# Kernel optimization log

Measured on AMD Instinct MI355X. Metric: run time of the kernel, lower is better.

The kernel has to match this reference:

```python
import jax, jax.numpy as jnp
import numpy as np

EPS = 1e-12  # F.normalize default eps


def setup_inputs() -> dict:
    key = jax.random.key(0)
    x = jax.random.normal(key, (10000, 512), dtype=jnp.float32)
    return {"x": x, "k": 9}


def reference(x, k):
    # F.normalize(x, p=2, dim=0): L2-normalize each feature column over points
    col_norm = jnp.sqrt(jnp.sum(x * x, axis=0, keepdims=True))  # [1, D]
    xn = x / jnp.maximum(col_norm, EPS)                          # [N, D]

    # pairwise squared euclidean distance: ||xi||^2 - 2 xi.xj + ||xj||^2
    sq = jnp.sum(xn * xn, axis=-1, keepdims=True)                # [N, 1]
    dist = sq - 2.0 * (xn @ xn.T) + sq.T                          # [N, N]

    # k nearest neighbors = top-k of negative distance
    _, nn_idx = jax.lax.top_k(-dist, k)                           # [N, k] int32

    n = x.shape[0]
    center_idx = jnp.broadcast_to(jnp.arange(n, dtype=nn_idx.dtype)[:, None], (n, k))
    edge_idx = jnp.stack((nn_idx, center_idx), axis=0)            # [2, N, k]
    return edge_idx
```

## Files before the change

### kernel.cpp

```cpp
#include <hip/hip_runtime.h>
#include <math.h>

#define DD 512
#define NBLKA 400

#define PM 128
#define PN 128
#define KB 64
#define CSPLIT 6
#define NC 12
#define PBUF 32
#define PBSTRIDE 36
#define NCTOT (CSPLIT*NC)
#define KOUTMAX 16
#define RS_MARGIN 2e-4f

typedef __attribute__((ext_vector_type(8))) short bf16x8;
typedef __attribute__((ext_vector_type(4))) float f32x4;

static __device__ __forceinline__ unsigned short f2bf(float f) {
    unsigned u = __float_as_uint(f);
    u += 0x7fff + ((u >> 16) & 1);
    return (unsigned short)(u >> 16);
}

__global__ void colsum_partial(const float* __restrict__ x, double* __restrict__ partial,
                               int N, int rows_per_block) {
    int b = blockIdx.x;
    int t = threadIdx.x;
    int r0 = b * rows_per_block;
    int r1 = min(r0 + rows_per_block, N);
    double s0 = 0.0, s1 = 0.0;
    for (int r = r0; r < r1; ++r) {
        float v0 = x[(size_t)r * DD + t];
        float v1 = x[(size_t)r * DD + t + 256];
        s0 += (double)v0 * (double)v0;
        s1 += (double)v1 * (double)v1;
    }
    partial[(size_t)b * DD + t]       = s0;
    partial[(size_t)b * DD + t + 256] = s1;
}

__global__ void colnorm_finish(const double* __restrict__ partial, double* __restrict__ rn,
                               double* __restrict__ w, int nblk) {
    int c = threadIdx.x;
    double s = 0.0;
    for (int b = 0; b < nblk; ++b) s += partial[(size_t)b * DD + c];
    double n = fmax(sqrt(s), 1e-12);
    double r = 1.0 / n;
    rn[c]  = r;
    w[c]   = r * r;
}

__global__ void row_sq(const float* __restrict__ x, const double* __restrict__ rn,
                       double* __restrict__ sq, float* __restrict__ sqf,
                       unsigned short* __restrict__ xnbf, int N) {
    int i = blockIdx.x;
    int t = threadIdx.x;
    double a0 = (double)x[(size_t)i * DD + t]       * rn[t];
    double a1 = (double)x[(size_t)i * DD + t + 256] * rn[t + 256];
    xnbf[(size_t)i * DD + t]       = f2bf((float)a0);
    xnbf[(size_t)i * DD + t + 256] = f2bf((float)a1);
    double local = a0 * a0 + a1 * a1;
    __shared__ double red[256];
    red[t] = local;
    __syncthreads();
    for (int off = 128; off > 0; off >>= 1) {
        if (t < off) red[t] += red[t + off];
        __syncthreads();
    }
    if (t == 0) { sq[i] = red[0]; sqf[i] = (float)red[0]; }
}

__global__ __launch_bounds__(256, 2) void gemm_prefilter(
    const unsigned short* __restrict__ xnbf,
    const float* __restrict__ sqf, int* __restrict__ cand, float* __restrict__ cands,
    int N, int ntileM, int ntileN)
{
    __shared__ __align__(16) unsigned char lds_raw[65536];
    __shared__ float sqi_s[PM];
    __shared__ float sqj_s[PN];
    __shared__ float thr_s[PM];
    __shared__ int   cnt_s[PM];
    __shared__ int   flag_s;

    float (*Bsc)[PBSTRIDE] = (float (*)[PBSTRIDE]) lds_raw;
    int   (*Bid)[PBSTRIDE] = (int   (*)[PBSTRIDE]) (lds_raw + 32768);

    const int bid   = blockIdx.x;
    const int q     = bid & 7;
    const int s     = bid >> 3;
    const int ridx  = s / CSPLIT;
    const int split = s - ridx * CSPLIT;
    const int rowb  = q + 8 * ridx;
    if (rowb >= ntileM) return;
    const int row0  = rowb * PM;

    const int t      = threadIdx.x;
    const int lane15 = t & 15;
    const int quad   = (t >> 4) & 3;
    const int wave   = t >> 6;
    const int wr     = (wave >> 1) * 64;
    const int wc     = (wave & 1) * 64;

    if (t == 0) flag_s = 0;
    if (t < PM) {
        int i = row0 + t;
        sqi_s[t] = (i < N) ? sqf[i] : 0.f;
        thr_s[t] = __builtin_inff();
        cnt_s[t] = 0;
    }

    float ls[NC];
    int   li[NC];
#pragma unroll
    for (int m = 0; m < NC; ++m) { ls[m] = __builtin_inff(); li[m] = 0x7fffffff; }

    f32x4 acc[4][4];

    for (int tile = split; tile < ntileN; tile += CSPLIT) {
        int col0 = tile * PN;

        if (t < PN) {
            int j = col0 + t;
            sqj_s[t] = (j < N) ? sqf[j] : __builtin_inff();
        }
        __syncthreads();

#pragma unroll
        for (int mt = 0; mt < 4; ++mt)
#pragma unroll
            for (int nt = 0; nt < 4; ++nt)
                acc[mt][nt] = (f32x4){0.f, 0.f, 0.f, 0.f};

        auto STAGE = [&](int kc, int buf) {
#pragma unroll
            for (int l = 0; l < 4; ++l) {
                int e    = t + l * 256;
                int half = e >> 9;
                int re   = e & 511;
                int row  = re >> 2;
                int c    = re & 3;
                size_t gA = (size_t)(row0 + row) * DD + kc + half * 32 + c * 8;
                __builtin_amdgcn_global_load_lds(
                    (const unsigned int*)(xnbf + gA),
                    (unsigned int*)(lds_raw + (size_t)buf * 16384 + (size_t)e * 16), 16, 0, 0);
                size_t gB = (size_t)(col0 + row) * DD + kc + half * 32 + c * 8;
                __builtin_amdgcn_global_load_lds(
                    (const unsigned int*)(xnbf + gB),
                    (unsigned int*)(lds_raw + 32768 + (size_t)buf * 16384 + (size_t)e * 16), 16, 0, 0);
            }
        };

        STAGE(0, 0);
#pragma unroll 1
        for (int cc = 0; cc < 8; ++cc) {
            if (cc < 7) {
                STAGE((cc + 1) * KB, (cc + 1) & 1);
                __builtin_amdgcn_sched_barrier(0);
                asm volatile("s_waitcnt vmcnt(8)" ::: "memory");
            } else {
                __builtin_amdgcn_sched_barrier(0);
                asm volatile("s_waitcnt vmcnt(0)" ::: "memory");
            }
            __builtin_amdgcn_s_barrier();
            __builtin_amdgcn_sched_barrier(0);

            const unsigned short (*Ab)[PM][32] =
                (const unsigned short (*)[PM][32])(lds_raw + (size_t)(cc & 1) * 16384);
            const unsigned short (*Bb)[PN][32] =
                (const unsigned short (*)[PN][32])(lds_raw + 32768 + (size_t)(cc & 1) * 16384);
#pragma unroll
            for (int ks = 0; ks < 2; ++ks) {
                bf16x8 af[4], bfg[4];
#pragma unroll
                for (int mt = 0; mt < 4; ++mt)
                    af[mt] = *(const bf16x8*)&Ab[ks][wr + mt * 16 + lane15][quad * 8];
#pragma unroll
                for (int nt = 0; nt < 4; ++nt)
                    bfg[nt] = *(const bf16x8*)&Bb[ks][wc + nt * 16 + lane15][quad * 8];
#pragma unroll
                for (int mt = 0; mt < 4; ++mt)
#pragma unroll
                    for (int nt = 0; nt < 4; ++nt)
                        acc[mt][nt] = __builtin_amdgcn_mfma_f32_16x16x32_bf16(
                            af[mt], bfg[nt], acc[mt][nt], 0, 0, 0);
            }
            __builtin_amdgcn_sched_barrier(0);
            __builtin_amdgcn_s_barrier();
        }

#pragma unroll
        for (int mt = 0; mt < 4; ++mt)
#pragma unroll
            for (int nt = 0; nt < 4; ++nt)
#pragma unroll
                for (int reg = 0; reg < 4; ++reg) {
                    int rl = wr + mt * 16 + quad * 4 + reg;
                    int cl = wc + nt * 16 + lane15;
                    float g = acc[mt][nt][reg];
                    acc[mt][nt][reg] = (sqi_s[rl] - 2.f * g) + sqj_s[cl];
                }

        bool tile_edge = (col0 + PN > N);
        unsigned long long done = 0ull;
        for (;;) {
#pragma unroll
            for (int mt = 0; mt < 4; ++mt)
#pragma unroll
                for (int reg = 0; reg < 4; ++reg) {
                    const unsigned long long gb =
                        (0x1111ull << reg) << (mt * 16);
                    int rl = wr + mt * 16 + quad * 4 + reg;
                    float th = thr_s[rl];
                    float gmin = fminf(fminf(acc[mt][0][reg], acc[mt][1][reg]),
                                       fminf(acc[mt][2][reg], acc[mt][3][reg]));
                    if (!tile_edge && gmin > th) { done |= gb; continue; }
                    if ((done & gb) == gb) continue;
#pragma unroll
                    for (int nt = 0; nt < 4; ++nt) {
                        const unsigned long long bit = 1ull << (mt * 16 + nt * 4 + reg);
                        if (!(done & bit)) {
                            float sv = acc[mt][nt][reg];
                            int   j  = col0 + wc + nt * 16 + lane15;
                            if (j < N && sv <= th) {
                                int pos = atomicAdd(&cnt_s[rl], 1);
                                if (pos < PBUF) {
                                    Bsc[rl][pos] = sv;
                                    Bid[rl][pos] = j;
                                    done |= bit;
                                }
                            } else {
                                done |= bit;
                            }
                        }
                    }
                }
            if (done != ~0ull) flag_s = 1;
            __syncthreads();
            if (t < PM) {
                int c = cnt_s[t];
                if (c > PBUF) c = PBUF;
                cnt_s[t] = 0;
                for (int m0 = 0; m0 < c; m0 += 4) {
                    float4 s4 = *(const float4*)&Bsc[t][m0];
                    int4   j4 = *(const int4*)&Bid[t][m0];
#pragma unroll
                    for (int e = 0; e < 4; ++e) {
                        if (m0 + e >= c) break;
                        float sv = (e == 0) ? s4.x : (e == 1) ? s4.y : (e == 2) ? s4.z : s4.w;
                        int   j  = (e == 0) ? j4.x : (e == 1) ? j4.y : (e == 2) ? j4.z : j4.w;
                        if (sv < ls[NC - 1] || (sv == ls[NC - 1] && j < li[NC - 1])) {
                            float cs = sv; int cj = j;
#pragma unroll
                            for (int p = 0; p < NC; ++p) {
                                bool lt = (cs < ls[p]) || (cs == ls[p] && cj < li[p]);
                                float ts = ls[p]; int tj = li[p];
                                if (lt) { ls[p] = cs; li[p] = cj; cs = ts; cj = tj; }
                            }
                        }
                    }
                }
                thr_s[t] = ls[NC - 1];
            }
            __syncthreads();
            int go = flag_s;
            __syncthreads();
            if (t == 0) flag_s = 0;
            __syncthreads();
            if (!go) break;
        }
    }
    if (t < PM) {
        int i = row0 + t;
        if (i < N) {
#pragma unroll
            for (int m = 0; m < NC; ++m) {
                cand [(size_t)i * NCTOT + split * NC + m] = li[m];
                cands[(size_t)i * NCTOT + split * NC + m] = ls[m];
            }
        }
    }
}

__global__ __launch_bounds__(256) void rescore_topk(
    const float* __restrict__ x, const double* __restrict__ w,
    const double* __restrict__ sq, const int* __restrict__ cand,
    const float* __restrict__ cands, int* __restrict__ out, int N, int k)
{
    __shared__ float Ssc[4][NCTOT];
    int lane = threadIdx.x & 63;
    int wid  = threadIdx.x >> 6;
    int i = blockIdx.x * 4 + wid;
    if (i >= N) return;

    size_t base = (size_t)i * NCTOT;
    Ssc[wid][lane] = cands[base + lane];
    if (lane < NCTOT - 64) Ssc[wid][64 + lane] = cands[base + 64 + lane];

    float p0 = Ssc[wid][lane];
    float p1 = Ssc[wid][64 + (lane & 7)];
    int c0 = 0, c1 = 0;
    for (int m = 0; m < NCTOT; ++m) {
        float s = Ssc[wid][m];
        c0 += (s <= p0); c1 += (s <= p1);
    }
    float best = __builtin_inff();
    if (c0 >= k) best = p0;
    if (c1 >= k && p1 < best) best = p1;
#pragma unroll
    for (int off = 32; off > 0; off >>= 1)
        best = fminf(best, __shfl_xor(best, off, 64));
    float cut = best + RS_MARGIN;

    double aw[8];
#pragma unroll
    for (int c = 0; c < 8; ++c) {
        int d = lane + 64 * c;
        aw[c] = (double)x[(size_t)i * DD + d] * w[d];
    }
    double sqi = sq[i];

    double bs[KOUTMAX];
    int    bj[KOUTMAX];
    for (int r = 0; r < k; ++r) { bs[r] = __builtin_inf(); bj[r] = 0x7fffffff; }

    int pend = -1;
    for (int m = 0; m <= NCTOT; ++m) {
        int j1cand = -1;
        if (m < NCTOT) {
            if (Ssc[wid][m] > cut) continue;
            j1cand = cand[base + m];
            if (pend < 0) { pend = j1cand; continue; }
        } else if (pend < 0) {
            break;
        }
        int j0 = pend, j1 = j1cand;
        pend = -1;
        const float* q0 = &x[(size_t)j0 * DD + lane];
        const float* q1 = (j1 >= 0) ? &x[(size_t)j1 * DD + lane] : q0;
        float v0[8], v1[8];
#pragma unroll
        for (int c = 0; c < 8; ++c) v0[c] = q0[64 * c];
#pragma unroll
        for (int c = 0; c < 8; ++c) v1[c] = q1[64 * c];
        double d0 = 0.0, d1 = 0.0;
#pragma unroll
        for (int c = 0; c < 8; ++c) d0 = fma(aw[c], (double)v0[c], d0);
#pragma unroll
        for (int c = 0; c < 8; ++c) d1 = fma(aw[c], (double)v1[c], d1);
#pragma unroll
        for (int off = 32; off > 0; off >>= 1) {
            d0 += __shfl_xor(d0, off, 64);
            d1 += __shfl_xor(d1, off, 64);
        }
        double s0 = (sqi - 2.0 * d0) + sq[j0];
        double s1 = (j1 >= 0) ? (sqi - 2.0 * d1) + sq[j1] : __builtin_inf();
#pragma unroll 1
        for (int pick = 0; pick < 2; ++pick) {
            double sv = pick ? s1 : s0;
            int    j  = pick ? j1 : j0;
            if (j < 0) continue;
            if (sv < bs[k - 1] || (sv == bs[k - 1] && j < bj[k - 1])) {
                int pos = k - 1;
                while (pos > 0) {
                    double ps = bs[pos - 1]; int pj = bj[pos - 1];
                    if (!(sv < ps || (sv == ps && j < pj))) break;
                    bs[pos] = ps; bj[pos] = pj;
                    --pos;
                }
                bs[pos] = sv; bj[pos] = j;
            }
        }
    }
    if (lane == 0) {
        for (int r = 0; r < k; ++r) {
            out[(size_t)i * k + r]                 = bj[r];
            out[(size_t)N * k + (size_t)i * k + r] = i;
        }
    }
}

extern "C" void kernel_launch(void* const* d_in, const int* in_sizes, int n_in,
                              void* d_out, int out_size, void* d_ws, size_t ws_size,
                              hipStream_t stream) {
    const float* x = (const float*)d_in[0];
    int N = in_sizes[0] / DD;
    int k = out_size / (2 * N);
    if (k > KOUTMAX) k = KOUTMAX;

    char* ws = (char*)d_ws;
    double*         partial = (double*)ws;
    double*         rn      = (double*)(ws + 1638400);
    double*         w       = (double*)(ws + 1642496);
    double*         sq      = (double*)(ws + 1646592);
    float*          sqf     = (float*) (ws + 1726592);
    unsigned short* xnbf    = (unsigned short*)(ws + 1766592);
    int*            cand    = (int*)   (ws + 12006592);
    float*          cands   = (float*) (ws + 14886592);

    int rpb = (N + NBLKA - 1) / NBLKA;
    hipLaunchKernelGGL(colsum_partial, dim3(NBLKA), dim3(256), 0, stream, x, partial, N, rpb);
    hipLaunchKernelGGL(colnorm_finish, dim3(1), dim3(512), 0, stream, partial, rn, w, NBLKA);
    hipLaunchKernelGGL(row_sq, dim3(N), dim3(256), 0, stream, x, rn, sq, sqf, xnbf, N);

    int ntileM = (N + PM - 1) / PM;
    int ntileN = (N + PN - 1) / PN;
    int rows_per_xcd = (ntileM + 7) / 8;
    int nblk = 8 * rows_per_xcd * CSPLIT;
    hipLaunchKernelGGL(gemm_prefilter, dim3(nblk), dim3(256), 0, stream,
                       xnbf, sqf, cand, cands, N, ntileM, ntileN);

    hipLaunchKernelGGL(rescore_topk, dim3((N + 3) / 4), dim3(256), 0, stream,
                       x, w, sq, cand, cands, (int*)d_out, N, k);
}
```

Before: 774.0 us.

## Keep per-row top-candidate lists in registers with transposed MFMA tiling

Restructures the GEMM prefilter so each wave owns 32 query rows across all 128 columns, swapping MFMA operand order so each lane holds distance values for a single query row. Candidates are inserted directly into per-lane register top-NC lists and then merged across quads with xor shuffles. This replaces the LDS buffer, atomic counters and multi-barrier retry loop. It also drops the row-norm term, which is constant per row and does not change the ranking, and adds an XOR swizzle to the LDS staging layout to reduce bank conflicts. The cost is more registers per thread for two candidate lists plus the accumulators, and insertion work that is serialized per lane.

```diff
diff --git a/kernel.cpp b/kernel.cpp
--- a/kernel.cpp
+++ b/kernel.cpp
@@ -9,8 +9,6 @@
 #define KB 64
 #define CSPLIT 6
 #define NC 12
-#define PBUF 32
-#define PBSTRIDE 36
 #define NCTOT (CSPLIT*NC)
 #define KOUTMAX 16
 #define RS_MARGIN 2e-4f
@@ -23,6 +21,19 @@
     u += 0x7fff + ((u >> 16) & 1);
     return (unsigned short)(u >> 16);
 }
+
+#define INSERT_CAND(LS, LI, SV, JJ)                                           \
+    do {                                                                      \
+        if ((SV) < LS[NC-1] || ((SV) == LS[NC-1] && (JJ) < LI[NC-1])) {       \
+            float cs_ = (SV); int cj_ = (JJ);                                 \
+            _Pragma("unroll")                                                 \
+            for (int p_ = 0; p_ < NC; ++p_) {                                 \
+                bool lt_ = (cs_ < LS[p_]) || (cs_ == LS[p_] && cj_ < LI[p_]); \
+                float ts_ = LS[p_]; int tj_ = LI[p_];                         \
+                if (lt_) { LS[p_] = cs_; LI[p_] = cj_; cs_ = ts_; cj_ = tj_; }\
+            }                                                                 \
+        }                                                                     \
+    } while (0)
 
 __global__ void colsum_partial(const float* __restrict__ x, double* __restrict__ partial,
                                int N, int rows_per_block) {
@@ -78,14 +89,7 @@
     int N, int ntileM, int ntileN)
 {
     __shared__ __align__(16) unsigned char lds_raw[65536];
-    __shared__ float sqi_s[PM];
     __shared__ float sqj_s[PN];
-    __shared__ float thr_s[PM];
-    __shared__ int   cnt_s[PM];
-    __shared__ int   flag_s;
-
-    float (*Bsc)[PBSTRIDE] = (float (*)[PBSTRIDE]) lds_raw;
-    int   (*Bid)[PBSTRIDE] = (int   (*)[PBSTRIDE]) (lds_raw + 32768);
 
     const int bid   = blockIdx.x;
     const int q     = bid & 7;
@@ -100,23 +104,19 @@
     const int lane15 = t & 15;
     const int quad   = (t >> 4) & 3;
     const int wave   = t >> 6;
-    const int wr     = (wave >> 1) * 64;
-    const int wc     = (wave & 1) * 64;
-
-    if (t == 0) flag_s = 0;
-    if (t < PM) {
-        int i = row0 + t;
-        sqi_s[t] = (i < N) ? sqf[i] : 0.f;
-        thr_s[t] = __builtin_inff();
-        cnt_s[t] = 0;
-    }
-
-    float ls[NC];
-    int   li[NC];
-#pragma unroll
-    for (int m = 0; m < NC; ++m) { ls[m] = __builtin_inff(); li[m] = 0x7fffffff; }
-
-    f32x4 acc[4][4];
+    const int i0     = wave * 32;
+    const int rg4    = quad * 4;
+    const int cq8    = (quad ^ (lane15 & 3)) * 8;
+
+    float ls0[NC], ls1[NC];
+    int   li0[NC], li1[NC];
+#pragma unroll
+    for (int m = 0; m < NC; ++m) {
+        ls0[m] = __builtin_inff(); li0[m] = 0x7fffffff;
+        ls1[m] = __builtin_inff(); li1[m] = 0x7fffffff;
+    }
+
+    f32x4 acc[8][2];
 
     for (int tile = split; tile < ntileN; tile += CSPLIT) {
         int col0 = tile * PN;
@@ -128,10 +128,10 @@
         __syncthreads();
 
 #pragma unroll
-        for (int mt = 0; mt < 4; ++mt)
-#pragma unroll
-            for (int nt = 0; nt < 4; ++nt)
-                acc[mt][nt] = (f32x4){0.f, 0.f, 0.f, 0.f};
+        for (int jt = 0; jt < 8; ++jt)
+#pragma unroll
+            for (int it = 0; it < 2; ++it)
+                acc[jt][it] = (f32x4){0.f, 0.f, 0.f, 0.f};
 
         auto STAGE = [&](int kc, int buf) {
 #pragma unroll
@@ -140,7 +140,7 @@
                 int half = e >> 9;
                 int re   = e & 511;
                 int row  = re >> 2;
-                int c    = re & 3;
+                int c    = (re & 3) ^ (row & 3);
                 size_t gA = (size_t)(row0 + row) * DD + kc + half * 32 + c * 8;
                 __builtin_amdgcn_global_load_lds(
                     (const unsigned int*)(xnbf + gA),
@@ -172,112 +172,93 @@
                 (const unsigned short (*)[PN][32])(lds_raw + 32768 + (size_t)(cc & 1) * 16384);
 #pragma unroll
             for (int ks = 0; ks < 2; ++ks) {
-                bf16x8 af[4], bfg[4];
-#pragma unroll
-                for (int mt = 0; mt < 4; ++mt)
-                    af[mt] = *(const bf16x8*)&Ab[ks][wr + mt * 16 + lane15][quad * 8];
-#pragma unroll
-                for (int nt = 0; nt < 4; ++nt)
-                    bfg[nt] = *(const bf16x8*)&Bb[ks][wc + nt * 16 + lane15][quad * 8];
-#pragma unroll
-                for (int mt = 0; mt < 4; ++mt)
-#pragma unroll
-                    for (int nt = 0; nt < 4; ++nt)
-                        acc[mt][nt] = __builtin_amdgcn_mfma_f32_16x16x32_bf16(
-                            af[mt], bfg[nt], acc[mt][nt], 0, 0, 0);
+                bf16x8 bj[8], ai[2];
+#pragma unroll
+                for (int jt = 0; jt < 8; ++jt)
+                    bj[jt] = *(const bf16x8*)&Bb[ks][jt * 16 + lane15][cq8];
+#pragma unroll
+                for (int it = 0; it < 2; ++it)
+                    ai[it] = *(const bf16x8*)&Ab[ks][i0 + it * 16 + lane15][cq8];
+#pragma unroll
+                for (int jt = 0; jt < 8; ++jt)
+#pragma unroll
+                    for (int it = 0; it < 2; ++it)
+                        acc[jt][it] = __builtin_amdgcn_mfma_f32_16x16x32_bf16(
+                            bj[jt], ai[it], acc[jt][it], 0, 0, 0);
             }
             __builtin_amdgcn_sched_barrier(0);
             __builtin_amdgcn_s_barrier();
         }
 
 #pragma unroll
-        for (int mt = 0; mt < 4; ++mt)
-#pragma unroll
-            for (int nt = 0; nt < 4; ++nt)
-#pragma unroll
-                for (int reg = 0; reg < 4; ++reg) {
-                    int rl = wr + mt * 16 + quad * 4 + reg;
-                    int cl = wc + nt * 16 + lane15;
-                    float g = acc[mt][nt][reg];
-                    acc[mt][nt][reg] = (sqi_s[rl] - 2.f * g) + sqj_s[cl];
+        for (int jt = 0; jt < 8; ++jt) {
+            const float4 sq4 = *(const float4*)&sqj_s[jt * 16 + rg4];
+            const int jb = col0 + jt * 16 + rg4;
+            {
+                float s0 = fmaf(-2.f, acc[jt][0][0], sq4.x);
+                float s1 = fmaf(-2.f, acc[jt][0][1], sq4.y);
+                float s2 = fmaf(-2.f, acc[jt][0][2], sq4.z);
+                float s3 = fmaf(-2.f, acc[jt][0][3], sq4.w);
+                float mn = fminf(fminf(s0, s1), fminf(s2, s3));
+                if (mn <= ls0[NC - 1]) {
+                    if (jb + 0 < N) INSERT_CAND(ls0, li0, s0, jb + 0);
+                    if (jb + 1 < N) INSERT_CAND(ls0, li0, s1, jb + 1);
+                    if (jb + 2 < N) INSERT_CAND(ls0, li0, s2, jb + 2);
+                    if (jb + 3 < N) INSERT_CAND(ls0, li0, s3, jb + 3);
                 }
-
-        bool tile_edge = (col0 + PN > N);
-        unsigned long long done = 0ull;
-        for (;;) {
-#pragma unroll
-            for (int mt = 0; mt < 4; ++mt)
-#pragma unroll
-                for (int reg = 0; reg < 4; ++reg) {
-                    const unsigned long long gb =
-                        (0x1111ull << reg) << (mt * 16);
-                    int rl = wr + mt * 16 + quad * 4 + reg;
-                    float th = thr_s[rl];
-                    float gmin = fminf(fminf(acc[mt][0][reg], acc[mt][1][reg]),
-                                       fminf(acc[mt][2][reg], acc[mt][3][reg]));
-                    if (!tile_edge && gmin > th) { done |= gb; continue; }
-                    if ((done & gb) == gb) continue;
-#pragma unroll
-                    for (int nt = 0; nt < 4; ++nt) {
-                        const unsigned long long bit = 1ull << (mt * 16 + nt * 4 + reg);
-                        if (!(done & bit)) {
-                            float sv = acc[mt][nt][reg];
-                            int   j  = col0 + wc + nt * 16 + lane15;
-                            if (j < N && sv <= th) {
-                                int pos = atomicAdd(&cnt_s[rl], 1);
-                                if (pos < PBUF) {
-                                    Bsc[rl][pos] = sv;
-                                    Bid[rl][pos] = j;
-                                    done |= bit;
-                                }
-                            } else {
-                                done |= bit;
-                            }
-                        }
-                    }
+            }
+            {
+                float s0 = fmaf(-2.f, acc[jt][1][0], sq4.x);
+                float s1 = fmaf(-2.f, acc[jt][1][1], sq4.y);
+                float s2 = fmaf(-2.f, acc[jt][1][2], sq4.z);
+                float s3 = fmaf(-2.f, acc[jt][1][3], sq4.w);
+                float mn = fminf(fminf(s0, s1), fminf(s2, s3));
+                if (mn <= ls1[NC - 1]) {
+                    if (jb + 0 < N) INSERT_CAND(ls1, li1, s0, jb + 0);
+                    if (jb + 1 < N) INSERT_CAND(ls1, li1, s1, jb + 1);
+                    if (jb + 2 < N) INSERT_CAND(ls1, li1, s2, jb + 2);
+                    if (jb + 3 < N) INSERT_CAND(ls1, li1, s3, jb + 3);
                 }
-            if (done != ~0ull) flag_s = 1;
-            __syncthreads();
-            if (t < PM) {
-                int c = cnt_s[t];
-                if (c > PBUF) c = PBUF;
-                cnt_s[t] = 0;
-                for (int m0 = 0; m0 < c; m0 += 4) {
-                    float4 s4 = *(const float4*)&Bsc[t][m0];
-                    int4   j4 = *(const int4*)&Bid[t][m0];
-#pragma unroll
-                    for (int e = 0; e < 4; ++e) {
-                        if (m0 + e >= c) break;
-                        float sv = (e == 0) ? s4.x : (e == 1) ? s4.y : (e == 2) ? s4.z : s4.w;
-                        int   j  = (e == 0) ? j4.x : (e == 1) ? j4.y : (e == 2) ? j4.z : j4.w;
-                        if (sv < ls[NC - 1] || (sv == ls[NC - 1] && j < li[NC - 1])) {
-                            float cs = sv; int cj = j;
-#pragma unroll
-                            for (int p = 0; p < NC; ++p) {
-                                bool lt = (cs < ls[p]) || (cs == ls[p] && cj < li[p]);
-                                float ts = ls[p]; int tj = li[p];
-                                if (lt) { ls[p] = cs; li[p] = cj; cs = ts; cj = tj; }
-                            }
-                        }
-                    }
-                }
-                thr_s[t] = ls[NC - 1];
-            }
-            __syncthreads();
-            int go = flag_s;
-            __syncthreads();
-            if (t == 0) flag_s = 0;
-            __syncthreads();
-            if (!go) break;
-        }
-    }
-    if (t < PM) {
-        int i = row0 + t;
-        if (i < N) {
+            }
+        }
+        __syncthreads();
+    }
+
+#pragma unroll
+    for (int r = 0; r < 2; ++r) {
+        const int msk = r ? 32 : 16;
+        float os[NC]; int oi[NC];
+#pragma unroll
+        for (int e = 0; e < NC; ++e) {
+            os[e] = __shfl_xor(ls0[e], msk, 64);
+            oi[e] = __shfl_xor(li0[e], msk, 64);
+        }
+#pragma unroll
+        for (int e = 0; e < NC; ++e) INSERT_CAND(ls0, li0, os[e], oi[e]);
+#pragma unroll
+        for (int e = 0; e < NC; ++e) {
+            os[e] = __shfl_xor(ls1[e], msk, 64);
+            oi[e] = __shfl_xor(li1[e], msk, 64);
+        }
+#pragma unroll
+        for (int e = 0; e < NC; ++e) INSERT_CAND(ls1, li1, os[e], oi[e]);
+    }
+
+    if (quad == 0) {
+        int ii0 = row0 + i0 + lane15;
+        if (ii0 < N) {
 #pragma unroll
             for (int m = 0; m < NC; ++m) {
-                cand [(size_t)i * NCTOT + split * NC + m] = li[m];
-                cands[(size_t)i * NCTOT + split * NC + m] = ls[m];
+                cand [(size_t)ii0 * NCTOT + split * NC + m] = li0[m];
+                cands[(size_t)ii0 * NCTOT + split * NC + m] = ls0[m];
+            }
+        }
+        int ii1 = row0 + i0 + 16 + lane15;
+        if (ii1 < N) {
+#pragma unroll
+            for (int m = 0; m < NC; ++m) {
+                cand [(size_t)ii1 * NCTOT + split * NC + m] = li1[m];
+                cands[(size_t)ii1 * NCTOT + split * NC + m] = ls1[m];
             }
         }
     }
```

After: 1.306 ms. 68.7% more time.

## Give each wave private LDS staging regions and drop per-chunk block barriers

Applied to the files above, without the earlier changes.

Each wave now stages only its own 64 rows of A and 64 columns of B into a private LDS region, with KB halved to 32 and twice as many chunks. This removes both workgroup-wide s_barriers from every K-chunk. The LDS layout uses an XOR swizzle on the 16-byte column slot to avoid bank conflicts. The trade-off is redundant global loads, since waves sharing rows or columns each fetch them separately. There are also more loop iterations, and the vmcnt(8) wait now applies to a smaller pipeline depth.

```diff
diff --git a/kernel.cpp b/kernel.cpp
--- a/kernel.cpp
+++ b/kernel.cpp
@@ -6,7 +6,7 @@
 
 #define PM 128
 #define PN 128
-#define KB 64
+#define KB 32
 #define CSPLIT 6
 #define NC 12
 #define PBUF 32
@@ -97,11 +97,14 @@
     const int row0  = rowb * PM;
 
     const int t      = threadIdx.x;
+    const int lane   = t & 63;
     const int lane15 = t & 15;
     const int quad   = (t >> 4) & 3;
     const int wave   = t >> 6;
     const int wr     = (wave >> 1) * 64;
     const int wc     = (wave & 1) * 64;
+    unsigned char* wreg = lds_raw + (size_t)wave * 16384;
+    const int sl     = quad ^ (lane15 & 3);
 
     if (t == 0) flag_s = 0;
     if (t < PM) {
@@ -133,29 +136,28 @@
             for (int nt = 0; nt < 4; ++nt)
                 acc[mt][nt] = (f32x4){0.f, 0.f, 0.f, 0.f};
 
-        auto STAGE = [&](int kc, int buf) {
+        auto STAGE = [&](int kc, int h) {
+            unsigned char* base = wreg + (size_t)h * 8192;
 #pragma unroll
             for (int l = 0; l < 4; ++l) {
-                int e    = t + l * 256;
-                int half = e >> 9;
-                int re   = e & 511;
-                int row  = re >> 2;
-                int c    = re & 3;
-                size_t gA = (size_t)(row0 + row) * DD + kc + half * 32 + c * 8;
+                int e = l * 64 + lane;
+                int r = e >> 2;
+                int c = (e & 3) ^ (r & 3);
+                size_t gA = (size_t)(row0 + wr + r) * DD + kc + c * 8;
                 __builtin_amdgcn_global_load_lds(
                     (const unsigned int*)(xnbf + gA),
-                    (unsigned int*)(lds_raw + (size_t)buf * 16384 + (size_t)e * 16), 16, 0, 0);
-                size_t gB = (size_t)(col0 + row) * DD + kc + half * 32 + c * 8;
+                    (unsigned int*)(base + (size_t)e * 16), 16, 0, 0);
+                size_t gB = (size_t)(col0 + wc + r) * DD + kc + c * 8;
                 __builtin_amdgcn_global_load_lds(
                     (const unsigned int*)(xnbf + gB),
-                    (unsigned int*)(lds_raw + 32768 + (size_t)buf * 16384 + (size_t)e * 16), 16, 0, 0);
+                    (unsigned int*)(base + 4096 + (size_t)e * 16), 16, 0, 0);
             }
         };
 
         STAGE(0, 0);
 #pragma unroll 1
-        for (int cc = 0; cc < 8; ++cc) {
-            if (cc < 7) {
+        for (int cc = 0; cc < 16; ++cc) {
+            if (cc < 15) {
                 STAGE((cc + 1) * KB, (cc + 1) & 1);
                 __builtin_amdgcn_sched_barrier(0);
                 asm volatile("s_waitcnt vmcnt(8)" ::: "memory");
@@ -163,31 +165,23 @@
                 __builtin_amdgcn_sched_barrier(0);
                 asm volatile("s_waitcnt vmcnt(0)" ::: "memory");
             }
-            __builtin_amdgcn_s_barrier();
             __builtin_amdgcn_sched_barrier(0);
 
-            const unsigned short (*Ab)[PM][32] =
-                (const unsigned short (*)[PM][32])(lds_raw + (size_t)(cc & 1) * 16384);
-            const unsigned short (*Bb)[PN][32] =
-                (const unsigned short (*)[PN][32])(lds_raw + 32768 + (size_t)(cc & 1) * 16384);
-#pragma unroll
-            for (int ks = 0; ks < 2; ++ks) {
-                bf16x8 af[4], bfg[4];
-#pragma unroll
-                for (int mt = 0; mt < 4; ++mt)
-                    af[mt] = *(const bf16x8*)&Ab[ks][wr + mt * 16 + lane15][quad * 8];
+            const unsigned char* rb = wreg + (size_t)(cc & 1) * 8192;
+            bf16x8 af[4], bfg[4];
+#pragma unroll
+            for (int mt = 0; mt < 4; ++mt)
+                af[mt] = *(const bf16x8*)(rb + ((size_t)((mt * 16 + lane15) * 4 + sl)) * 16);
+#pragma unroll
+            for (int nt = 0; nt < 4; ++nt)
+                bfg[nt] = *(const bf16x8*)(rb + 4096 + ((size_t)((nt * 16 + lane15) * 4 + sl)) * 16);
+#pragma unroll
+            for (int mt = 0; mt < 4; ++mt)
 #pragma unroll
                 for (int nt = 0; nt < 4; ++nt)
-                    bfg[nt] = *(const bf16x8*)&Bb[ks][wc + nt * 16 + lane15][quad * 8];
-#pragma unroll
-                for (int mt = 0; mt < 4; ++mt)
-#pragma unroll
-                    for (int nt = 0; nt < 4; ++nt)
-                        acc[mt][nt] = __builtin_amdgcn_mfma_f32_16x16x32_bf16(
-                            af[mt], bfg[nt], acc[mt][nt], 0, 0, 0);
-            }
+                    acc[mt][nt] = __builtin_amdgcn_mfma_f32_16x16x32_bf16(
+                        af[mt], bfg[nt], acc[mt][nt], 0, 0, 0);
             __builtin_amdgcn_sched_barrier(0);
-            __builtin_amdgcn_s_barrier();
         }
 
 #pragma unroll
@@ -201,6 +195,7 @@
                     float g = acc[mt][nt][reg];
                     acc[mt][nt][reg] = (sqi_s[rl] - 2.f * g) + sqj_s[cl];
                 }
+        __syncthreads();
 
         bool tile_edge = (col0 + PN > N);
         unsigned long long done = 0ull;
```

After: 802.2 us. 3.6% more time.
